# Optimization experiments

Measured on AMD Instinct MI355X. Metric: run time of the kernel, lower is better.

## Reference

```python
import jax, jax.numpy as jnp
import numpy as np

NUM_HEADS = 32
NUM_KV_HEADS = 8
HEAD_DIM = 128
HIDDEN = 4096
THETA = 10000.0


def apply_rotary_emb(x, theta=THETA):
    # x: (B, S, H, D). Torch code converts to complex with real = first half
    # of last dim, imag = second half (rotate-half convention).
    B, S, H, D = x.shape
    half = D // 2
    freqs = 1.0 / theta ** (jnp.arange(0, D, 2, dtype=jnp.float32) / D)  # (half,)
    t = jnp.arange(S, dtype=jnp.float32)
    ang = jnp.outer(t, freqs)  # (S, half)
    cos = jnp.cos(ang)[None, :, None, :]  # (1,S,1,half)
    sin = jnp.sin(ang)[None, :, None, :]
    x1, x2 = x[..., :half], x[..., half:]
    out = jnp.concatenate([x1 * cos - x2 * sin, x1 * sin + x2 * cos], axis=-1)
    return out.astype(x.dtype)


def setup_inputs() -> dict:
    key = jax.random.key(0)
    k1, k2, k3 = jax.random.split(key, 3)
    B, S = 1, 2048
    qkv_out = (NUM_HEADS + 2 * NUM_KV_HEADS) * HEAD_DIM  # 6144
    hidden_states = jax.random.normal(k1, (B, S, HIDDEN), dtype=jnp.float32)
    w_qkv = jax.random.normal(k2, (qkv_out, HIDDEN), dtype=jnp.float32) * 0.02
    w_o = jax.random.normal(k3, (HIDDEN, NUM_HEADS * HEAD_DIM), dtype=jnp.float32) * 0.02
    return {"hidden_states": hidden_states, "w_qkv": w_qkv, "w_o": w_o}


def reference(hidden_states, w_qkv, w_o):
    B, S, _ = hidden_states.shape
    q_size = NUM_HEADS * HEAD_DIM
    kv_size = NUM_KV_HEADS * HEAD_DIM
    n_rep = NUM_HEADS // NUM_KV_HEADS

    qkv = hidden_states @ w_qkv.T  # (B,S,6144)
    xq = qkv[..., :q_size].reshape(B, S, NUM_HEADS, HEAD_DIM)
    xk = qkv[..., q_size:q_size + kv_size].reshape(B, S, NUM_KV_HEADS, HEAD_DIM)
    xv = qkv[..., q_size + kv_size:].reshape(B, S, NUM_KV_HEADS, HEAD_DIM)

    xq = apply_rotary_emb(xq)
    xk = apply_rotary_emb(xk)

    # repeat_interleave KV heads to match query heads
    xk = jnp.repeat(xk, n_rep, axis=2)
    xv = jnp.repeat(xv, n_rep, axis=2)

    q = xq.transpose(0, 2, 1, 3)  # (B,H,S,D)
    k = xk.transpose(0, 2, 1, 3)
    v = xv.transpose(0, 2, 1, 3)

    scale = 1.0 / np.sqrt(HEAD_DIM).astype(np.float32)
    scores = jnp.einsum('bhqd,bhkd->bhqk', q, k) * scale
    causal = jnp.tril(jnp.ones((S, S), dtype=bool))
    scores = jnp.where(causal[None, None], scores, jnp.float32(-jnp.inf))
    attn = jax.nn.softmax(scores, axis=-1)  # dropout=0 (eval)
    out = jnp.einsum('bhqk,bhkd->bhqd', attn, v)
    out = out.transpose(0, 2, 1, 3).reshape(B, S, NUM_HEADS * HEAD_DIM)
    return out @ w_o.T
```

## Files before the change

kernel.cpp:

```cpp
#include <hip/hip_runtime.h>
#include <cstdint>

#define S_LEN 2048
#define HID   4096
#define NHQ   32
#define NKV   8
#define HD    128
#define QKV_N 6144

typedef float  f32x4 __attribute__((ext_vector_type(4)));
typedef short  s16x8 __attribute__((ext_vector_type(8)));
typedef unsigned short ushort_t;

typedef __attribute__((address_space(3))) void       lds_void;
typedef const __attribute__((address_space(1))) void gbl_void;

__device__ __forceinline__ void gload_lds16(const void* g, void* l) {
  __builtin_amdgcn_global_load_lds((gbl_void*)g, (lds_void*)l, 16, 0, 0);
}

__device__ __forceinline__ short f2bf_bits(float f) {
  union { __bf16 b; short s; } u;
  u.b = (__bf16)f;
  return u.s;
}
__device__ __forceinline__ float bf2f(unsigned short u) {
  union { unsigned int i; float f; } x;
  x.i = ((unsigned int)u) << 16;
  return x.f;
}

__device__ __forceinline__ void cvt8(const float* src, ushort_t* dst, int j) {
  const f32x4* s = (const f32x4*)src;
  f32x4 a = s[j * 2], b = s[j * 2 + 1];
  s16x8 r;
  r[0] = f2bf_bits(a[0]); r[1] = f2bf_bits(a[1]); r[2] = f2bf_bits(a[2]); r[3] = f2bf_bits(a[3]);
  r[4] = f2bf_bits(b[0]); r[5] = f2bf_bits(b[1]); r[6] = f2bf_bits(b[2]); r[7] = f2bf_bits(b[3]);
  *((s16x8*)dst + j) = r;
}

__global__ __launch_bounds__(256)
void cvt_hw(const float* __restrict__ h, const float* __restrict__ wq,
            ushort_t* __restrict__ hb, ushort_t* __restrict__ wqb) {
  int i = blockIdx.x * 256 + threadIdx.x;
  if (i < 1048576) cvt8(h, hb, i);
  else             cvt8(wq, wqb, i - 1048576);
}

__device__ __forceinline__ s16x8 frag_b16(const ushort_t* tile, int row, int quad) {
  return *(const s16x8*)(tile + row * 32 + quad * 8);
}

template <bool OUTF32>
__global__ __launch_bounds__(256)
void gemm_bt_bf16(const ushort_t* __restrict__ Ag, const ushort_t* __restrict__ Bg,
                  void* __restrict__ Cp, int M, int N, int K) {
  __shared__ __align__(16) ushort_t As[2][128 * 32];
  __shared__ __align__(16) ushort_t Bs[2][128 * 32];
  const int t = threadIdx.x;
  const int w = t >> 6, l = t & 63;
  const int n16 = l & 15, quad = l >> 4;
  const int m0 = blockIdx.x * 128, n0 = blockIdx.y * 128;
  const int wm = (w >> 1) * 64, wn = (w & 1) * 64;

  const int sIdx0 = (w * 2 + 0) * 64 + l;
  const int sIdx1 = (w * 2 + 1) * 64 + l;
  const int aRow0 = sIdx0 >> 2, aCs0 = (sIdx0 & 3) * 8;
  const int aRow1 = sIdx1 >> 2, aCs1 = (sIdx1 & 3) * 8;
  const ushort_t* Arow0 = Ag + (size_t)(m0 + aRow0) * K + aCs0;
  const ushort_t* Arow1 = Ag + (size_t)(m0 + aRow1) * K + aCs1;
  const ushort_t* Brow0 = Bg + (size_t)(n0 + aRow0) * K + aCs0;
  const ushort_t* Brow1 = Bg + (size_t)(n0 + aRow1) * K + aCs1;

  f32x4 acc[4][4] = {};

  auto stage = [&](int k0, int buf) {
    gload_lds16(Arow0 + k0, (char*)&As[buf][0] + (w * 2 + 0) * 1024);
    gload_lds16(Arow1 + k0, (char*)&As[buf][0] + (w * 2 + 1) * 1024);
    gload_lds16(Brow0 + k0, (char*)&Bs[buf][0] + (w * 2 + 0) * 1024);
    gload_lds16(Brow1 + k0, (char*)&Bs[buf][0] + (w * 2 + 1) * 1024);
  };
  auto compute = [&](int buf) {
    s16x8 afr[4], bfr[4];
#pragma unroll
    for (int i = 0; i < 4; i++) afr[i] = frag_b16(&As[buf][0], wm + i * 16 + n16, quad);
#pragma unroll
    for (int j = 0; j < 4; j++) bfr[j] = frag_b16(&Bs[buf][0], wn + j * 16 + n16, quad);
#pragma unroll
    for (int i = 0; i < 4; i++)
#pragma unroll
      for (int j = 0; j < 4; j++)
        acc[i][j] = __builtin_amdgcn_mfma_f32_16x16x32_bf16(afr[i], bfr[j], acc[i][j], 0, 0, 0);
  };

  const int nIter = K >> 5;
  stage(0, 0);
  for (int it = 0; it < nIter; it += 2) {
    __syncthreads();
    if (it + 1 < nIter) stage((it + 1) << 5, 1);
    compute(0);
    __syncthreads();
    if (it + 2 < nIter) stage((it + 2) << 5, 0);
    compute(1);
  }

#pragma unroll
  for (int i = 0; i < 4; i++)
#pragma unroll
    for (int j = 0; j < 4; j++)
#pragma unroll
      for (int r = 0; r < 4; r++) {
        int row = m0 + wm + i * 16 + quad * 4 + r;
        int col = n0 + wn + j * 16 + n16;
        float v = acc[i][j][r];
        if constexpr (OUTF32) ((float*)Cp)[(size_t)row * N + col] = v;
        else ((ushort_t*)Cp)[(size_t)row * N + col] = (ushort_t)f2bf_bits(v);
      }
}

__global__ __launch_bounds__(256)
void rope_vt_cvtwo(const ushort_t* __restrict__ qkv, ushort_t* __restrict__ Q,
                   ushort_t* __restrict__ Kc, ushort_t* __restrict__ Vt,
                   const float* __restrict__ wo, ushort_t* __restrict__ wob) {
  __shared__ __align__(16) ushort_t tile[64][72];
  const int b = blockIdx.x;
  const int t = threadIdx.x;
  if (b < 2048) {
    const int s = b;
    const float LN1E4_64 = 0.14391156831212787f;
    for (int item = t; item < (NHQ + NKV) * 64; item += 256) {
      int head = item >> 6, i = item & 63;
      float f = expf(-(float)i * LN1E4_64);
      float ang = (float)s * f;
      float sn, cs;
      sincosf(ang, &sn, &cs);
      if (head < NHQ) {
        const ushort_t* src = qkv + (size_t)s * QKV_N + head * HD;
        float x1 = bf2f(src[i]), x2 = bf2f(src[64 + i]);
        const float sc = 0.08838834764831845f;
        ushort_t* dst = Q + ((size_t)head * S_LEN + s) * HD;
        dst[i]      = (ushort_t)f2bf_bits((x1 * cs - x2 * sn) * sc);
        dst[64 + i] = (ushort_t)f2bf_bits((x1 * sn + x2 * cs) * sc);
      } else {
        int kv = head - NHQ;
        const ushort_t* src = qkv + (size_t)s * QKV_N + 4096 + kv * HD;
        float x1 = bf2f(src[i]), x2 = bf2f(src[64 + i]);
        ushort_t* dst = Kc + ((size_t)kv * S_LEN + s) * HD;
        dst[i]      = (ushort_t)f2bf_bits(x1 * cs - x2 * sn);
        dst[64 + i] = (ushort_t)f2bf_bits(x1 * sn + x2 * cs);
      }
    }
  } else if (b < 2560) {
    const int bb = b - 2048;
    const int s0 = (bb & 31) * 64;
    const int by = bb >> 5;
    const int kv = by >> 1;
    const int d0 = (by & 1) * 64;
    {
      int r = t >> 2, c = (t & 3) * 16;
      const ushort_t* src = qkv + (size_t)(s0 + r) * QKV_N + 5120 + kv * HD + d0 + c;
      *(s16x8*)&tile[r][c]     = *(const s16x8*)src;
      *(s16x8*)&tile[r][c + 8] = *(const s16x8*)(src + 8);
    }
    __syncthreads();
    {
      int d = t >> 2, sseg = (t & 3) * 16;
      ushort_t* dst = Vt + ((size_t)kv * HD + d0 + d) * S_LEN + s0 + sseg;
      s16x8 o1, o2;
#pragma unroll
      for (int i = 0; i < 8; i++) { o1[i] = tile[sseg + i][d]; o2[i] = tile[sseg + 8 + i][d]; }
      *(s16x8*)dst = o1;
      *(s16x8*)(dst + 8) = o2;
    }
  } else {
    int j = (b - 2560) * 256 + t;
    cvt8(wo, wob, j);
  }
}

__global__ __launch_bounds__(256)
void attn_kernel(const ushort_t* __restrict__ Q, const ushort_t* __restrict__ Kc,
                 const ushort_t* __restrict__ Vt, ushort_t* __restrict__ Out) {
  __shared__ __align__(16) ushort_t Ks[2][64 * 128];
  __shared__ __align__(16) ushort_t Vs[2][128 * 64];
  __shared__ __align__(16) ushort_t Pl[4][16 * 72];
  const int bx = blockIdx.x;
  const int h = blockIdx.y;
  const int t = threadIdx.x, w = t >> 6, l = t & 63;
  const int n16 = l & 15, quad = l >> 4;
  const int kv = h >> 2;
  const ushort_t* Qh = Q  + (size_t)h  * S_LEN * HD;
  const ushort_t* Kh = Kc + (size_t)kv * S_LEN * HD;
  const ushort_t* Vh = Vt + (size_t)kv * HD * S_LEN;

  const int qtA = bx, qtB = 31 - bx;
  const int q0A = qtA * 64 + w * 16, q0B = qtB * 64 + w * 16;
  const int tripsA = qtA + 1;
  const int TOTAL = 33;

  s16x8 qfA[4], qfB[4];
#pragma unroll
  for (int ks = 0; ks < 4; ks++) {
    qfA[ks] = *(const s16x8*)(Qh + (size_t)(q0A + n16) * HD + ks * 32 + quad * 8);
    qfB[ks] = *(const s16x8*)(Qh + (size_t)(q0B + n16) * HD + ks * 32 + quad * 8);
  }

  s16x8 ones;
  {
    short v = (n16 == 0) ? (short)0x3F80 : (short)0;
#pragma unroll
    for (int j = 0; j < 8; j++) ones[j] = v;
  }

  f32x4 o[9] = {};
  float mrun[4] = {-1e30f, -1e30f, -1e30f, -1e30f};

  ushort_t* P = Pl[w];

  auto stage = [&](int k0, int buf) {
#pragma unroll
    for (int c = 0; c < 4; c++) {
      int idx = (c * 4 + w) * 64 + l;
      int row = idx >> 4, sc = idx & 15;
      int dseg = sc ^ (row & 15);
      gload_lds16(Kh + (size_t)(k0 + row) * HD + dseg * 8,
                  (char*)&Ks[buf][0] + (c * 4 + w) * 1024);
    }
#pragma unroll
    for (int c = 0; c < 4; c++) {
      int idx = (c * 4 + w) * 64 + l;
      int row = idx >> 3, sc = idx & 7;
      int ks2 = sc ^ (row & 7);
      gload_lds16(Vh + (size_t)row * S_LEN + k0 + ks2 * 8,
                  (char*)&Vs[buf][0] + (c * 4 + w) * 1024);
    }
  };

  stage(0, 0);

  for (int i = 0; i < TOTAL; i++) {
    const bool isA = (i < tripsA);
    const int kt = isA ? i : i - tripsA;
    const int q0 = isA ? q0A : q0B;
    const int k0 = kt * 64;
    const int buf = i & 1;

    __syncthreads();

    if (i + 1 < TOTAL) {
      const bool nA = (i + 1 < tripsA);
      const int nkt = nA ? (i + 1) : (i + 1 - tripsA);
      stage(nkt * 64, buf ^ 1);
    }

    const ushort_t* KsB = &Ks[buf][0];
    const ushort_t* VsB = &Vs[buf][0];

    f32x4 sacc[4] = {};
    __builtin_amdgcn_s_setprio(1);
#pragma unroll
    for (int ks = 0; ks < 4; ks++) {
      s16x8 qf = isA ? qfA[ks] : qfB[ks];
#pragma unroll
      for (int nt = 0; nt < 4; nt++) {
        int row = nt * 16 + n16;
        s16x8 kf = *(const s16x8*)(KsB + row * 128 + ((ks * 4 + quad) ^ (row & 15)) * 8);
        sacc[nt] = __builtin_amdgcn_mfma_f32_16x16x32_bf16(qf, kf, sacc[nt], 0, 0, 0);
      }
    }
    __builtin_amdgcn_s_setprio(0);

    if (k0 + 63 > q0) {
#pragma unroll
      for (int nt = 0; nt < 4; nt++)
#pragma unroll
        for (int r = 0; r < 4; r++) {
          int qrow = q0 + quad * 4 + r;
          int key  = k0 + nt * 16 + n16;
          if (key > qrow) sacc[nt][r] = -1e30f;
        }
    }

    float tmx[4];
    int need = 0;
#pragma unroll
    for (int r = 0; r < 4; r++) {
      float tm = fmaxf(fmaxf(sacc[0][r], sacc[1][r]), fmaxf(sacc[2][r], sacc[3][r]));
#pragma unroll
      for (int d = 1; d < 16; d <<= 1) tm = fmaxf(tm, __shfl_xor(tm, d));
      tmx[r] = tm;
      need |= (tm > mrun[r] + 8.0f) ? 1 : 0;
    }
    if (__any(need)) {
#pragma unroll
      for (int r = 0; r < 4; r++) {
        float nm = fmaxf(mrun[r], tmx[r]);
        float alpha = __expf(mrun[r] - nm);
        mrun[r] = nm;
#pragma unroll
        for (int nt2 = 0; nt2 < 9; nt2++) o[nt2][r] *= alpha;
      }
    }
#pragma unroll
    for (int r = 0; r < 4; r++)
#pragma unroll
      for (int nt = 0; nt < 4; nt++) sacc[nt][r] = __expf(sacc[nt][r] - mrun[r]);

#pragma unroll
    for (int nt = 0; nt < 4; nt++)
#pragma unroll
      for (int r = 0; r < 4; r++)
        P[(quad * 4 + r) * 72 + nt * 16 + n16] = (ushort_t)f2bf_bits(sacc[nt][r]);
    asm volatile("s_waitcnt lgkmcnt(0)" ::: "memory");
    s16x8 pa[2];
#pragma unroll
    for (int kseg = 0; kseg < 2; kseg++)
      pa[kseg] = *(const s16x8*)(P + n16 * 72 + kseg * 32 + quad * 8);

    __builtin_amdgcn_s_setprio(1);
#pragma unroll
    for (int kseg = 0; kseg < 2; kseg++) {
#pragma unroll
      for (int ntd = 0; ntd < 8; ntd++) {
        int row = ntd * 16 + n16;
        s16x8 vf = *(const s16x8*)(VsB + row * 64 + ((kseg * 4 + quad) ^ (row & 7)) * 8);
        o[ntd] = __builtin_amdgcn_mfma_f32_16x16x32_bf16(pa[kseg], vf, o[ntd], 0, 0, 0);
      }
      o[8] = __builtin_amdgcn_mfma_f32_16x16x32_bf16(pa[kseg], ones, o[8], 0, 0, 0);
    }
    __builtin_amdgcn_s_setprio(0);

    if (i == tripsA - 1) {
#pragma unroll
      for (int r = 0; r < 4; r++) {
        float lsum = __shfl(o[8][r], l & 48);
        float inv = 1.0f / lsum;
        int qrow = q0A + quad * 4 + r;
#pragma unroll
        for (int ntd = 0; ntd < 8; ntd++)
          Out[(size_t)qrow * HID + h * HD + ntd * 16 + n16] = (ushort_t)f2bf_bits(o[ntd][r] * inv);
      }
#pragma unroll
      for (int nt2 = 0; nt2 < 9; nt2++) o[nt2] = (f32x4){0.f, 0.f, 0.f, 0.f};
#pragma unroll
      for (int r = 0; r < 4; r++) mrun[r] = -1e30f;
    }
  }

#pragma unroll
  for (int r = 0; r < 4; r++) {
    float lsum = __shfl(o[8][r], l & 48);
    float inv = 1.0f / lsum;
    int qrow = q0B + quad * 4 + r;
#pragma unroll
    for (int ntd = 0; ntd < 8; ntd++)
      Out[(size_t)qrow * HID + h * HD + ntd * 16 + n16] = (ushort_t)f2bf_bits(o[ntd][r] * inv);
  }
}

extern "C" void kernel_launch(void* const* d_in, const int* in_sizes, int n_in,
                              void* d_out, int out_size, void* d_ws, size_t ws_size,
                              hipStream_t stream) {
  const float* hidden = (const float*)d_in[0];
  const float* w_qkv  = (const float*)d_in[1];
  const float* w_o    = (const float*)d_in[2];
  float* out = (float*)d_out;
  char* ws = (char*)d_ws;

  ushort_t* hidden_bf = (ushort_t*)ws;
  ushort_t* Qb        = (ushort_t*)ws;
  ushort_t* wqkv_bf   = (ushort_t*)(ws + 16777216);
  ushort_t* wo_bf     = (ushort_t*)(ws + 16777216);
  ushort_t* qkv       = (ushort_t*)(ws + 67108864);
  ushort_t* attn_out  = (ushort_t*)(ws + 67108864);
  ushort_t* Kb        = (ushort_t*)(ws + 92274688);
  ushort_t* Vtb       = (ushort_t*)(ws + 96468992);

  cvt_hw<<<dim3(16384), 256, 0, stream>>>(hidden, w_qkv, hidden_bf, wqkv_bf);
  gemm_bt_bf16<false><<<dim3(16, 48), 256, 0, stream>>>(hidden_bf, wqkv_bf, (void*)qkv, 2048, 6144, 4096);
  rope_vt_cvtwo<<<dim3(10752), 256, 0, stream>>>(qkv, Qb, Kb, Vtb, w_o, wo_bf);
  attn_kernel<<<dim3(16, 32), 256, 0, stream>>>(Qb, Kb, Vtb, attn_out);
  gemm_bt_bf16<true><<<dim3(16, 32), 256, 0, stream>>>(attn_out, wo_bf, (void*)out, 2048, 4096, 4096);
}
```

Baseline: 506.1 us.

## Split paired causal attention blocks into one q-tile per block with 32-key tiles

The attention kernel no longer pairs a short and a long query tile in one block. It launches 1024 blocks, one per (head, q-tile), ordered so that long and short tiles interleave across the grid, and it shrinks the key/value tiles from 64 to 32 rows so LDS use drops. Each wave also skips key tiles that lie wholly above its own causal diagonal. This gives more blocks for occupancy and finer causal skipping, at the cost of more barriers per key and a less even load per block.

```diff
diff --git a/kernel.cpp b/kernel.cpp
--- a/kernel.cpp
+++ b/kernel.cpp
@@ -181,169 +181,135 @@
 __global__ __launch_bounds__(256)
 void attn_kernel(const ushort_t* __restrict__ Q, const ushort_t* __restrict__ Kc,
                  const ushort_t* __restrict__ Vt, ushort_t* __restrict__ Out) {
-  __shared__ __align__(16) ushort_t Ks[2][64 * 128];
-  __shared__ __align__(16) ushort_t Vs[2][128 * 64];
-  __shared__ __align__(16) ushort_t Pl[4][16 * 72];
-  const int bx = blockIdx.x;
-  const int h = blockIdx.y;
+  __shared__ __align__(16) ushort_t Ks[2][32 * 128];
+  __shared__ __align__(16) ushort_t Vs[2][128 * 32];
+  __shared__ __align__(16) ushort_t Pl[4][16 * 32];
+  const int bidx = blockIdx.x;
+  const int g = bidx >> 8, rr = bidx & 255;
+  const int h = rr >> 3, j = rr & 7;
+  const int qt = (g == 0) ? j : (g == 1) ? (31 - j) : (g == 2) ? (8 + j) : (23 - j);
   const int t = threadIdx.x, w = t >> 6, l = t & 63;
   const int n16 = l & 15, quad = l >> 4;
   const int kv = h >> 2;
   const ushort_t* Qh = Q  + (size_t)h  * S_LEN * HD;
   const ushort_t* Kh = Kc + (size_t)kv * S_LEN * HD;
   const ushort_t* Vh = Vt + (size_t)kv * HD * S_LEN;
-
-  const int qtA = bx, qtB = 31 - bx;
-  const int q0A = qtA * 64 + w * 16, q0B = qtB * 64 + w * 16;
-  const int tripsA = qtA + 1;
-  const int TOTAL = 33;
-
-  s16x8 qfA[4], qfB[4];
-#pragma unroll
-  for (int ks = 0; ks < 4; ks++) {
-    qfA[ks] = *(const s16x8*)(Qh + (size_t)(q0A + n16) * HD + ks * 32 + quad * 8);
-    qfB[ks] = *(const s16x8*)(Qh + (size_t)(q0B + n16) * HD + ks * 32 + quad * 8);
-  }
+  const int q0 = qt * 64 + w * 16;
+  const int NT = 2 * qt + 2;
+
+  s16x8 qf[4];
+#pragma unroll
+  for (int ks = 0; ks < 4; ks++)
+    qf[ks] = *(const s16x8*)(Qh + (size_t)(q0 + n16) * HD + ks * 32 + quad * 8);
 
   s16x8 ones;
   {
     short v = (n16 == 0) ? (short)0x3F80 : (short)0;
 #pragma unroll
-    for (int j = 0; j < 8; j++) ones[j] = v;
+    for (int jj = 0; jj < 8; jj++) ones[jj] = v;
   }
 
   f32x4 o[9] = {};
   float mrun[4] = {-1e30f, -1e30f, -1e30f, -1e30f};
-
   ushort_t* P = Pl[w];
 
   auto stage = [&](int k0, int buf) {
 #pragma unroll
-    for (int c = 0; c < 4; c++) {
-      int idx = (c * 4 + w) * 64 + l;
+    for (int c = 0; c < 2; c++) {
+      int idx = c * 256 + t;
       int row = idx >> 4, sc = idx & 15;
       int dseg = sc ^ (row & 15);
       gload_lds16(Kh + (size_t)(k0 + row) * HD + dseg * 8,
-                  (char*)&Ks[buf][0] + (c * 4 + w) * 1024);
-    }
-#pragma unroll
-    for (int c = 0; c < 4; c++) {
-      int idx = (c * 4 + w) * 64 + l;
-      int row = idx >> 3, sc = idx & 7;
-      int ks2 = sc ^ (row & 7);
+                  (char*)&Ks[buf][0] + idx * 16);
+    }
+#pragma unroll
+    for (int c = 0; c < 2; c++) {
+      int idx = c * 256 + t;
+      int row = idx >> 2, sc = idx & 3;
+      int ks2 = sc ^ (row & 3);
       gload_lds16(Vh + (size_t)row * S_LEN + k0 + ks2 * 8,
-                  (char*)&Vs[buf][0] + (c * 4 + w) * 1024);
+                  (char*)&Vs[buf][0] + idx * 16);
     }
   };
 
   stage(0, 0);
 
-  for (int i = 0; i < TOTAL; i++) {
-    const bool isA = (i < tripsA);
-    const int kt = isA ? i : i - tripsA;
-    const int q0 = isA ? q0A : q0B;
-    const int k0 = kt * 64;
+  for (int i = 0; i < NT; i++) {
+    const int k0 = i * 32;
     const int buf = i & 1;
 
     __syncthreads();
-
-    if (i + 1 < TOTAL) {
-      const bool nA = (i + 1 < tripsA);
-      const int nkt = nA ? (i + 1) : (i + 1 - tripsA);
-      stage(nkt * 64, buf ^ 1);
-    }
-
-    const ushort_t* KsB = &Ks[buf][0];
-    const ushort_t* VsB = &Vs[buf][0];
-
-    f32x4 sacc[4] = {};
-    __builtin_amdgcn_s_setprio(1);
-#pragma unroll
-    for (int ks = 0; ks < 4; ks++) {
-      s16x8 qf = isA ? qfA[ks] : qfB[ks];
-#pragma unroll
-      for (int nt = 0; nt < 4; nt++) {
-        int row = nt * 16 + n16;
-        s16x8 kf = *(const s16x8*)(KsB + row * 128 + ((ks * 4 + quad) ^ (row & 15)) * 8);
-        sacc[nt] = __builtin_amdgcn_mfma_f32_16x16x32_bf16(qf, kf, sacc[nt], 0, 0, 0);
-      }
-    }
-    __builtin_amdgcn_s_setprio(0);
-
-    if (k0 + 63 > q0) {
-#pragma unroll
-      for (int nt = 0; nt < 4; nt++)
+    if (i + 1 < NT) stage((i + 1) * 32, buf ^ 1);
+
+    if (k0 <= q0 + 15) {
+      const ushort_t* KsB = &Ks[buf][0];
+      const ushort_t* VsB = &Vs[buf][0];
+
+      f32x4 sacc[2] = {};
+      __builtin_amdgcn_s_setprio(1);
+#pragma unroll
+      for (int ks = 0; ks < 4; ks++)
+#pragma unroll
+        for (int nt = 0; nt < 2; nt++) {
+          int row = nt * 16 + n16;
+          s16x8 kf = *(const s16x8*)(KsB + row * 128 + ((ks * 4 + quad) ^ (row & 15)) * 8);
+          sacc[nt] = __builtin_amdgcn_mfma_f32_16x16x32_bf16(qf[ks], kf, sacc[nt], 0, 0, 0);
+        }
+      __builtin_amdgcn_s_setprio(0);
+
+      if (k0 + 31 > q0) {
+#pragma unroll
+        for (int nt = 0; nt < 2; nt++)
+#pragma unroll
+          for (int r = 0; r < 4; r++) {
+            int qrow = q0 + quad * 4 + r;
+            int key  = k0 + nt * 16 + n16;
+            if (key > qrow) sacc[nt][r] = -1e30f;
+          }
+      }
+
+      int need = 0;
+#pragma unroll
+      for (int r = 0; r < 4; r++)
+#pragma unroll
+        for (int nt = 0; nt < 2; nt++)
+          need |= (sacc[nt][r] > mrun[r] + 8.0f) ? 1 : 0;
+      if (__any(need)) {
 #pragma unroll
         for (int r = 0; r < 4; r++) {
-          int qrow = q0 + quad * 4 + r;
-          int key  = k0 + nt * 16 + n16;
-          if (key > qrow) sacc[nt][r] = -1e30f;
+          float tm = fmaxf(sacc[0][r], sacc[1][r]);
+#pragma unroll
+          for (int d = 1; d < 16; d <<= 1) tm = fmaxf(tm, __shfl_xor(tm, d));
+          float nm = fmaxf(mrun[r], tm);
+          float alpha = __expf(mrun[r] - nm);
+          mrun[r] = nm;
+#pragma unroll
+          for (int nt2 = 0; nt2 < 9; nt2++) o[nt2][r] *= alpha;
         }
-    }
-
-    float tmx[4];
-    int need = 0;
-#pragma unroll
-    for (int r = 0; r < 4; r++) {
-      float tm = fmaxf(fmaxf(sacc[0][r], sacc[1][r]), fmaxf(sacc[2][r], sacc[3][r]));
-#pragma unroll
-      for (int d = 1; d < 16; d <<= 1) tm = fmaxf(tm, __shfl_xor(tm, d));
-      tmx[r] = tm;
-      need |= (tm > mrun[r] + 8.0f) ? 1 : 0;
-    }
-    if (__any(need)) {
-#pragma unroll
-      for (int r = 0; r < 4; r++) {
-        float nm = fmaxf(mrun[r], tmx[r]);
-        float alpha = __expf(mrun[r] - nm);
-        mrun[r] = nm;
-#pragma unroll
-        for (int nt2 = 0; nt2 < 9; nt2++) o[nt2][r] *= alpha;
-      }
-    }
-#pragma unroll
-    for (int r = 0; r < 4; r++)
-#pragma unroll
-      for (int nt = 0; nt < 4; nt++) sacc[nt][r] = __expf(sacc[nt][r] - mrun[r]);
-
-#pragma unroll
-    for (int nt = 0; nt < 4; nt++)
+      }
 #pragma unroll
       for (int r = 0; r < 4; r++)
-        P[(quad * 4 + r) * 72 + nt * 16 + n16] = (ushort_t)f2bf_bits(sacc[nt][r]);
-    asm volatile("s_waitcnt lgkmcnt(0)" ::: "memory");
-    s16x8 pa[2];
-#pragma unroll
-    for (int kseg = 0; kseg < 2; kseg++)
-      pa[kseg] = *(const s16x8*)(P + n16 * 72 + kseg * 32 + quad * 8);
-
-    __builtin_amdgcn_s_setprio(1);
-#pragma unroll
-    for (int kseg = 0; kseg < 2; kseg++) {
+#pragma unroll
+        for (int nt = 0; nt < 2; nt++)
+          sacc[nt][r] = __expf(sacc[nt][r] - mrun[r]);
+
+#pragma unroll
+      for (int nt = 0; nt < 2; nt++)
+#pragma unroll
+        for (int r = 0; r < 4; r++)
+          P[(quad * 4 + r) * 32 + nt * 16 + n16] = (ushort_t)f2bf_bits(sacc[nt][r]);
+      asm volatile("s_waitcnt lgkmcnt(0)" ::: "memory");
+      s16x8 pa = *(const s16x8*)(P + n16 * 32 + quad * 8);
+
+      __builtin_amdgcn_s_setprio(1);
 #pragma unroll
       for (int ntd = 0; ntd < 8; ntd++) {
         int row = ntd * 16 + n16;
-        s16x8 vf = *(const s16x8*)(VsB + row * 64 + ((kseg * 4 + quad) ^ (row & 7)) * 8);
-        o[ntd] = __builtin_amdgcn_mfma_f32_16x16x32_bf16(pa[kseg], vf, o[ntd], 0, 0, 0);
-      }
-      o[8] = __builtin_amdgcn_mfma_f32_16x16x32_bf16(pa[kseg], ones, o[8], 0, 0, 0);
-    }
-    __builtin_amdgcn_s_setprio(0);
-
-    if (i == tripsA - 1) {
-#pragma unroll
-      for (int r = 0; r < 4; r++) {
-        float lsum = __shfl(o[8][r], l & 48);
-        float inv = 1.0f / lsum;
-        int qrow = q0A + quad * 4 + r;
-#pragma unroll
-        for (int ntd = 0; ntd < 8; ntd++)
-          Out[(size_t)qrow * HID + h * HD + ntd * 16 + n16] = (ushort_t)f2bf_bits(o[ntd][r] * inv);
-      }
-#pragma unroll
-      for (int nt2 = 0; nt2 < 9; nt2++) o[nt2] = (f32x4){0.f, 0.f, 0.f, 0.f};
-#pragma unroll
-      for (int r = 0; r < 4; r++) mrun[r] = -1e30f;
+        s16x8 vf = *(const s16x8*)(VsB + row * 32 + ((quad ^ (row & 3))) * 8);
+        o[ntd] = __builtin_amdgcn_mfma_f32_16x16x32_bf16(pa, vf, o[ntd], 0, 0, 0);
+      }
+      o[8] = __builtin_amdgcn_mfma_f32_16x16x32_bf16(pa, ones, o[8], 0, 0, 0);
+      __builtin_amdgcn_s_setprio(0);
     }
   }
 
@@ -351,7 +317,7 @@
   for (int r = 0; r < 4; r++) {
     float lsum = __shfl(o[8][r], l & 48);
     float inv = 1.0f / lsum;
-    int qrow = q0B + quad * 4 + r;
+    int qrow = q0 + quad * 4 + r;
 #pragma unroll
     for (int ntd = 0; ntd < 8; ntd++)
       Out[(size_t)qrow * HID + h * HD + ntd * 16 + n16] = (ushort_t)f2bf_bits(o[ntd][r] * inv);
@@ -379,6 +345,6 @@
   cvt_hw<<<dim3(16384), 256, 0, stream>>>(hidden, w_qkv, hidden_bf, wqkv_bf);
   gemm_bt_bf16<false><<<dim3(16, 48), 256, 0, stream>>>(hidden_bf, wqkv_bf, (void*)qkv, 2048, 6144, 4096);
   rope_vt_cvtwo<<<dim3(10752), 256, 0, stream>>>(qkv, Qb, Kb, Vtb, w_o, wo_bf);
-  attn_kernel<<<dim3(16, 32), 256, 0, stream>>>(Qb, Kb, Vtb, attn_out);
+  attn_kernel<<<dim3(1024), 256, 0, stream>>>(Qb, Kb, Vtb, attn_out);
   gemm_bt_bf16<true><<<dim3(16, 32), 256, 0, stream>>>(attn_out, wo_bf, (void*)out, 2048, 4096, 4096);
 }
```

Result: no change. 502.6 us (-0.7%).
